# Kernel optimization log

Measured on AMD Instinct MI355X. Metric: run time of the kernel, lower is better.

The kernel has to match this reference:

```python
import jax, jax.numpy as jnp
import numpy as np
from itertools import product as _prod

B = 2          # batch size
NPB = 4096     # voxels per batch
C = 384        # input_dim
H = 8          # num_heads
OUT = 32       # output_dim (seg classes)
SPATIAL = (32, 256, 256)
POOL_R = np.array([1, 2, 2, 2])    # [1]+query_gs_ratio
COMP_R = np.array([1, 16, 16, 16])  # [1]+compress_ratio


def _coords():
    rng = np.random.default_rng(0)
    rows = []
    for b in range(B):
        cand = np.stack([rng.integers(0, s, 4 * NPB) for s in SPATIAL], 1)
        cand = np.unique(cand, axis=0)
        sel = cand[rng.permutation(len(cand))[:NPB]]
        rows.append(np.concatenate([np.full((NPB, 1), b, np.int64), sel], 1))
    return np.concatenate(rows).astype(np.int32)


def setup_inputs() -> dict:
    idx = _coords()                     # [N,4] unique (b,z,y,x)
    N = idx.shape[0]
    pool_u, pool_inv = np.unique(idx // POOL_R, axis=0, return_inverse=True)
    emb_u, emb_inv = np.unique(idx // COMP_R, axis=0, return_inverse=True)
    # submanifold 3x3x3 neighbor table (same batch), -1 = missing
    lut = {tuple(r): i for i, r in enumerate(idx.tolist())}
    nbr = np.full((N, 27), -1, np.int32)
    rows = idx.tolist()
    for k, (dz, dy, dx) in enumerate(_prod((-1, 0, 1), repeat=3)):
        for i, (b, z, y, x) in enumerate(rows):
            nbr[i, k] = lut.get((b, z + dz, y + dy, x + dx), -1)
    key = jax.random.key(0)
    ks = jax.random.split(key, 12)
    g = lambda k, shp, s: jax.random.normal(k, shp, jnp.float32) * s
    s = 1.0 / float(np.sqrt(C))
    return dict(
        feats=g(ks[0], (N, C), 1.0),
        W_pool=g(ks[1], (C, C), s), b_pool=jnp.zeros((C,), jnp.float32),
        W_emb=g(ks[2], (C, C), s), b_emb=jnp.zeros((C,), jnp.float32),
        Wq=g(ks[3], (C, C), s), bq=jnp.zeros((C,), jnp.float32),
        Wk=g(ks[4], (C, C), s), bk=jnp.zeros((C,), jnp.float32),
        Wv=g(ks[5], (C, C), s), bv=jnp.zeros((C,), jnp.float32),
        Wo=g(ks[6], (C, C), s), bo=jnp.zeros((C,), jnp.float32),
        W_conv=g(ks[7], (27, C, OUT), 1.0 / float(np.sqrt(27 * C))),
        b_conv=jnp.zeros((OUT,), jnp.float32),
        pool_inv=jnp.asarray(pool_inv, jnp.int32),
        pool_coords=jnp.asarray(pool_u, jnp.int32),
        emb_inv=jnp.asarray(emb_inv, jnp.int32),
        emb_coords=jnp.asarray(emb_u, jnp.int32),
        nbr_idx=jnp.asarray(nbr),
        batch_size=B,
    )


def _sine_pe(xyz, d_pos):
    # xyz: [n,3] normalized to [0,1]; PositionEmbeddingCoordsSine (3detr-style)
    cdim = d_pos // xyz.shape[1]
    dim_t = 10000.0 ** (2.0 * (jnp.arange(cdim) // 2).astype(jnp.float32) / cdim)
    emb = (xyz * (2.0 * jnp.pi))[:, :, None] / dim_t          # [n,3,cdim]
    pe = jnp.stack([jnp.sin(emb[..., 0::2]), jnp.cos(emb[..., 1::2])], -1)
    return pe.reshape(xyz.shape[0], -1)                        # [n,d_pos]


def reference(feats, W_pool, b_pool, W_emb, b_emb, Wq, bq, Wk, bk, Wv, bv,
              Wo, bo, W_conv, b_conv, pool_inv, pool_coords, emb_inv,
              emb_coords, nbr_idx, batch_size):
    Mp, Me, Cc = pool_coords.shape[0], emb_coords.shape[0], feats.shape[1]
    hd = Cc // H
    # query path: linear + scatter_max over pool cells
    pool_f = jax.ops.segment_max(feats @ W_pool + b_pool, pool_inv, num_segments=Mp)
    # kv path: linear + scatter_max over compressed cells (coords of argmax rows
    # within a cell all equal the unique cell coord, so mean == unique coord)
    emb_f = jax.ops.segment_max(feats @ W_emb + b_emb, emb_inv, num_segments=Me)
    # per-batch min/max-normalized sine positional encoding on concat(emb,pool)
    emb_xyz = emb_coords[:, 1:].astype(jnp.float32)
    pool_xyz = pool_coords[:, 1:].astype(jnp.float32)
    all_xyz = jnp.concatenate([emb_xyz, pool_xyz], 0)
    bids = jnp.concatenate([emb_coords[:, 0], pool_coords[:, 0]], 0)
    mins = jax.ops.segment_min(all_xyz, bids, num_segments=batch_size)
    maxs = jax.ops.segment_max(all_xyz, bids, num_segments=batch_size)
    norm = (all_xyz - mins[bids]) / (maxs[bids] - mins[bids] + 1e-6)
    pe = _sine_pe(norm, Cc)
    emb_f = emb_f + pe[:Me]
    pool_f = pool_f + pe[Me:]
    # multi-head cross-attention, masked to same-batch pairs
    q = (pool_f @ Wq + bq).reshape(Mp, H, hd)
    k = (emb_f @ Wk + bk).reshape(Me, H, hd)
    v = (emb_f @ Wv + bv).reshape(Me, H, hd)
    scores = jnp.einsum('phd,ehd->hpe', q, k) / jnp.sqrt(jnp.float32(hd))
    same_b = pool_coords[:, 0][None, :, None] == emb_coords[:, 0][None, None, :]
    attn = jax.nn.softmax(jnp.where(same_b, scores, -1e9), axis=-1)
    o = jnp.einsum('hpe,ehd->phd', attn, v).reshape(Mp, Cc) @ Wo + bo
    # broadcast back to voxels + residual
    new_f = feats + o[pool_inv]
    # SubMConv3d seg head: gather 27 neighbors, contract with kernel
    valid = (nbr_idx >= 0)[:, :, None]
    gathered = jnp.where(valid, new_f[jnp.maximum(nbr_idx, 0)], 0.0)  # [N,27,C]
    logits = jnp.einsum('nkc,kco->no', gathered, W_conv) + b_conv
    return logits
```

## Files before the change

### kernel.cpp

```cpp
#include <hip/hip_runtime.h>
#include <hip/hip_bf16.h>
#include <math.h>

#define CDIM 384
#define NHEAD 8
#define HD 48
#define OUTD 32
#define MAXB 16
#define CONVK 10368

typedef __bf16 bf16x8 __attribute__((ext_vector_type(8)));
typedef float f32x4 __attribute__((ext_vector_type(4)));

__device__ __forceinline__ f32x4 mfma16(bf16x8 a, bf16x8 b, f32x4 c) {
  return __builtin_amdgcn_mfma_f32_16x16x32_bf16(a, b, c, 0, 0, 0);
}
__device__ __forceinline__ bf16x8 zero8() {
  bf16x8 z = {(__bf16)0.f, (__bf16)0.f, (__bf16)0.f, (__bf16)0.f,
              (__bf16)0.f, (__bf16)0.f, (__bf16)0.f, (__bf16)0.f};
  return z;
}

__device__ __forceinline__ unsigned enc_f(float f) {
  unsigned u = __float_as_uint(f);
  return (u & 0x80000000u) ? ~u : (u | 0x80000000u);
}
__device__ __forceinline__ float dec_f(unsigned u) {
  unsigned v = (u & 0x80000000u) ? (u ^ 0x80000000u) : ~u;
  return __uint_as_float(v);
}

__global__ void init_small_kernel(int* smin, int* smax, int* eb) {
  int t = threadIdx.x;
  if (t < MAXB * 3) { smin[t] = 0x7fffffff; smax[t] = (int)0x80000000; }
  if (t <= MAXB) eb[t] = 0;
}

__global__ __launch_bounds__(256) void prep_kernel(
    const float* __restrict__ feats, __hip_bfloat16* __restrict__ feats16, int N,
    const float* __restrict__ W_pool, const float* __restrict__ W_emb,
    const float* __restrict__ Wk, const float* __restrict__ Wv,
    const float* __restrict__ Wq, const float* __restrict__ Wo,
    __hip_bfloat16* __restrict__ Wt_pe, __hip_bfloat16* __restrict__ Wt_kv,
    __hip_bfloat16* __restrict__ Wt_q, __hip_bfloat16* __restrict__ Wt_o,
    const float* __restrict__ Wc, __hip_bfloat16* __restrict__ Wct,
    unsigned* __restrict__ encA, unsigned* __restrict__ encB,
    __hip_bfloat16* __restrict__ vt, int Mepad,
    const int* __restrict__ ec, const int* __restrict__ pc, int Mp, int Me,
    const int* __restrict__ bsz, int* smin, int* smax, int* ebv,
    int nbF, int nbW, int nbC, int nbZA, int nbZB, int nbVt, int nbM) {
  __shared__ int lmin[MAXB * 3], lmax[MAXB * 3];
  int b = blockIdx.x;
  int t = threadIdx.x;
  if (b < nbF) {
    int v = b * 256 + t;
    if (v < N * 48) {
      float4 a0 = *reinterpret_cast<const float4*>(feats + (size_t)v * 8);
      float4 a1 = *reinterpret_cast<const float4*>(feats + (size_t)v * 8 + 4);
      __hip_bfloat16 tmp[8] = {
        __float2bfloat16(a0.x), __float2bfloat16(a0.y), __float2bfloat16(a0.z), __float2bfloat16(a0.w),
        __float2bfloat16(a1.x), __float2bfloat16(a1.y), __float2bfloat16(a1.z), __float2bfloat16(a1.w)};
      *reinterpret_cast<bf16x8*>(feats16 + (size_t)v * 8) = *reinterpret_cast<const bf16x8*>(tmp);
    }
    return;
  }
  b -= nbF;
  if (b < 6 * nbW) {
    int m = b / nbW;
    int v = (b - m * nbW) * 256 + t;
    if (v >= CDIM * 48) return;
    const float* src;
    __hip_bfloat16* dst;
    switch (m) {
      case 0: src = W_pool; dst = Wt_pe; break;
      case 1: src = W_emb;  dst = Wt_pe + (size_t)CDIM * CDIM; break;
      case 2: src = Wk;     dst = Wt_kv; break;
      case 3: src = Wv;     dst = Wt_kv + (size_t)CDIM * CDIM; break;
      case 4: src = Wq;     dst = Wt_q; break;
      default: src = Wo;    dst = Wt_o; break;
    }
    int k8i = v / CDIM;
    int n = v - k8i * CDIM;
    int k8 = k8i * 8;
    __hip_bfloat16 tmp[8];
    #pragma unroll
    for (int u = 0; u < 8; ++u) tmp[u] = __float2bfloat16(src[(size_t)(k8 + u) * CDIM + n]);
    *reinterpret_cast<bf16x8*>(dst + (size_t)n * CDIM + k8) = *reinterpret_cast<const bf16x8*>(tmp);
    return;
  }
  b -= 6 * nbW;
  if (b < nbC) {
    int v = b * 256 + t;
    if (v >= OUTD * (CONVK / 8)) return;
    int k8i = v >> 5;
    int n = v & 31;
    int k8 = k8i * 8;
    __hip_bfloat16 tmp[8];
    #pragma unroll
    for (int u = 0; u < 8; ++u) tmp[u] = __float2bfloat16(Wc[(size_t)(k8 + u) * OUTD + n]);
    *reinterpret_cast<bf16x8*>(Wct + (size_t)n * CONVK + k8) = *reinterpret_cast<const bf16x8*>(tmp);
    return;
  }
  b -= nbC;
  if (b < nbZA) {
    size_t v = (size_t)b * 256 + t;
    if (v < (size_t)Mp * 96) {
      uint4 z = {0u, 0u, 0u, 0u};
      reinterpret_cast<uint4*>(encA)[v] = z;
    }
    return;
  }
  b -= nbZA;
  if (b < nbZB) {
    size_t v = (size_t)b * 256 + t;
    if (v < (size_t)Me * 96) {
      uint4 z = {0u, 0u, 0u, 0u};
      reinterpret_cast<uint4*>(encB)[v] = z;
    }
    return;
  }
  b -= nbZB;
  if (b < nbVt) {
    int v = b * 256 + t;
    int g = Mepad >> 3;
    if (v < 512 * g) {
      int row = v / g;
      int c8 = (v - row * g) * 8;
      __hip_bfloat16 bv = __float2bfloat16(((row & 63) == HD) ? 1.0f : 0.0f);
      __hip_bfloat16 tmp[8] = {bv, bv, bv, bv, bv, bv, bv, bv};
      *reinterpret_cast<bf16x8*>(vt + (size_t)row * Mepad + c8) =
          *reinterpret_cast<const bf16x8*>(tmp);
    }
    return;
  }
  b -= nbVt;
  if (b < nbM) {
    if (t < MAXB * 3) { lmin[t] = 0x7fffffff; lmax[t] = (int)0x80000000; }
    __syncthreads();
    int i = b * 256 + t;
    int tot = Me + Mp;
    if (i < tot) {
      const int* r = (i < Me) ? (ec + 4 * i) : (pc + 4 * (i - Me));
      int bb = r[0];
      #pragma unroll
      for (int d = 0; d < 3; ++d) {
        atomicMin(&lmin[bb * 3 + d], r[1 + d]);
        atomicMax(&lmax[bb * 3 + d], r[1 + d]);
      }
    }
    __syncthreads();
    if (t < MAXB * 3) {
      if (lmin[t] != 0x7fffffff) atomicMin(&smin[t], lmin[t]);
      if (lmax[t] != (int)0x80000000) atomicMax(&smax[t], lmax[t]);
    }
    return;
  }
  b -= nbM;
  {
    int e = b * 256 + t;
    if (e == 0) { ebv[0] = 0; ebv[bsz[0]] = Me; }
    if (e > 0 && e < Me) {
      int b0 = ec[4 * (e - 1)], b1 = ec[4 * e];
      for (int bb = b0 + 1; bb <= b1; ++bb) ebv[bb] = e;
    }
  }
}

__global__ void pe_kernel(const unsigned* __restrict__ encP, const unsigned* __restrict__ encE,
                          __hip_bfloat16* __restrict__ pool16, __hip_bfloat16* __restrict__ emb16,
                          const int* __restrict__ pc, int Mp,
                          const int* __restrict__ ec, int Me,
                          const int* __restrict__ smin, const int* __restrict__ smax) {
  int gid = blockIdx.x * blockDim.x + threadIdx.x;
  int total = (Mp + Me) * CDIM;
  if (gid >= total) return;
  int row = gid / CDIM, c = gid - row * CDIM;
  const int* coords;
  const unsigned* src;
  __hip_bfloat16* dst;
  int lrow;
  if (row < Me) { lrow = row; coords = ec + 4 * row; src = encE; dst = emb16; }
  else { lrow = row - Me; coords = pc + 4 * lrow; src = encP; dst = pool16; }
  int b = coords[0];
  int dim = c >> 7;
  int i = c & 127;
  int j = i >> 1;
  float x = (float)coords[1 + dim];
  float mn = (float)smin[b * 3 + dim];
  float mx = (float)smax[b * 3 + dim];
  float nrm = (x - mn) / (mx - mn + 1e-6f);
  float freq = exp2f(-(float)j * 0.20762050593046014f);
  float arg = nrm * 6.283185307179586f * freq;
  float pe = (i & 1) ? __cosf(arg) : __sinf(arg);
  float val = dec_f(src[(size_t)lrow * CDIM + c]) + pe;
  dst[(size_t)lrow * CDIM + c] = __float2bfloat16(val);
}

template <int EPI>
__device__ __forceinline__ void mgemm_body(
    int bx, int by,
    __hip_bfloat16 (*As)[72], __hip_bfloat16 (*Bs)[72],
    const __hip_bfloat16* __restrict__ A, int M,
    const __hip_bfloat16* __restrict__ Wt,
    const float* __restrict__ bias0, const float* __restrict__ bias1,
    void* __restrict__ d0, void* __restrict__ d1,
    const int* __restrict__ inv0, const int* __restrict__ inv1,
    int Mepad) {
  const int m0 = bx * 128;
  const int n0 = by * 64;
  const int t = threadIdx.x;
  const int lane = t & 63, w = t >> 6;
  const int wr = w >> 1, wc = w & 1;
  const int lq = lane & 15, lg = lane >> 4;

  f32x4 acc[4][2];
  #pragma unroll
  for (int i = 0; i < 4; ++i) {
    acc[i][0] = (f32x4){0.f, 0.f, 0.f, 0.f};
    acc[i][1] = (f32x4){0.f, 0.f, 0.f, 0.f};
  }
  const int arow = t >> 3;
  const int acol = (t & 7) * 8;

  for (int k0 = 0; k0 < CDIM; k0 += 64) {
    #pragma unroll
    for (int i = 0; i < 4; ++i) {
      int r = arow + i * 32;
      int gr = m0 + r;
      bf16x8 val = zero8();
      if (gr < M) val = *reinterpret_cast<const bf16x8*>(A + (size_t)gr * CDIM + k0 + acol);
      *reinterpret_cast<bf16x8*>(&As[r][acol]) = val;
    }
    #pragma unroll
    for (int i = 0; i < 2; ++i) {
      int r = arow + i * 32;
      bf16x8 val = *reinterpret_cast<const bf16x8*>(Wt + (size_t)(n0 + r) * CDIM + k0 + acol);
      *reinterpret_cast<bf16x8*>(&Bs[r][acol]) = val;
    }
    __syncthreads();
    #pragma unroll
    for (int ks = 0; ks < 2; ++ks) {
      bf16x8 af[4], bfv[2];
      #pragma unroll
      for (int fm = 0; fm < 4; ++fm)
        af[fm] = *reinterpret_cast<const bf16x8*>(&As[wr * 64 + fm * 16 + lq][ks * 32 + lg * 8]);
      #pragma unroll
      for (int fn = 0; fn < 2; ++fn)
        bfv[fn] = *reinterpret_cast<const bf16x8*>(&Bs[wc * 32 + fn * 16 + lq][ks * 32 + lg * 8]);
      #pragma unroll
      for (int fm = 0; fm < 4; ++fm)
        #pragma unroll
        for (int fn = 0; fn < 2; ++fn)
          acc[fm][fn] = mfma16(af[fm], bfv[fn], acc[fm][fn]);
    }
    __syncthreads();
  }

  const bool sec = (n0 >= CDIM);
  const int nb = n0 - (sec ? CDIM : 0) + wc * 32;
  const int nA = nb + lq, nB = nb + 16 + lq;

  if (EPI == 0) {
    const float* bias = sec ? bias1 : bias0;
    unsigned* dst = (unsigned*)(sec ? d1 : d0);
    const int* inv = sec ? inv1 : inv0;
    float bA = bias[nA], bB = bias[nB];
    #pragma unroll
    for (int fm = 0; fm < 4; ++fm) {
      int rbase = m0 + wr * 64 + fm * 16 + lg * 4;
      int cs = -1;
      float mA = 0.f, mB = 0.f;
      #pragma unroll
      for (int j = 0; j < 4; ++j) {
        int r = rbase + j;
        if (r < M) {
          int s = inv[r];
          float vA = acc[fm][0][j] + bA;
          float vB = acc[fm][1][j] + bB;
          if (s == cs) { mA = fmaxf(mA, vA); mB = fmaxf(mB, vB); }
          else {
            if (cs >= 0) {
              atomicMax(&dst[(size_t)cs * CDIM + nA], enc_f(mA));
              atomicMax(&dst[(size_t)cs * CDIM + nB], enc_f(mB));
            }
            cs = s; mA = vA; mB = vB;
          }
        }
      }
      if (cs >= 0) {
        atomicMax(&dst[(size_t)cs * CDIM + nA], enc_f(mA));
        atomicMax(&dst[(size_t)cs * CDIM + nB], enc_f(mB));
      }
    }
  } else if (EPI == 1) {
    float bA = bias0[nA], bB = bias0[nB];
    float* dst = (float*)d0;
    #pragma unroll
    for (int fm = 0; fm < 4; ++fm)
      #pragma unroll
      for (int j = 0; j < 4; ++j) {
        int r = m0 + wr * 64 + fm * 16 + lg * 4 + j;
        if (r < M) {
          dst[(size_t)r * CDIM + nA] = acc[fm][0][j] + bA;
          dst[(size_t)r * CDIM + nB] = acc[fm][1][j] + bB;
        }
      }
  } else if (EPI == 2) {
    const float scale = 0.2082350914f;
    float bA = bias0[nA], bB = bias0[nB];
    int hA = nA / HD, dA = nA - hA * HD;
    int hB = nB / HD, dB = nB - hB * HD;
    __hip_bfloat16* dst = (__hip_bfloat16*)d0;
    #pragma unroll
    for (int fm = 0; fm < 4; ++fm)
      #pragma unroll
      for (int j = 0; j < 4; ++j) {
        int r = m0 + wr * 64 + fm * 16 + lg * 4 + j;
        if (r < M) {
          dst[(size_t)r * 512 + hA * 64 + dA] = __float2bfloat16((acc[fm][0][j] + bA) * scale);
          dst[(size_t)r * 512 + hB * 64 + dB] = __float2bfloat16((acc[fm][1][j] + bB) * scale);
        }
      }
  } else {
    if (!sec) {
      float bA = bias0[nA], bB = bias0[nB];
      int hA = nA / HD, dA = nA - hA * HD;
      int hB = nB / HD, dB = nB - hB * HD;
      __hip_bfloat16* dst = (__hip_bfloat16*)d0;
      #pragma unroll
      for (int fm = 0; fm < 4; ++fm)
        #pragma unroll
        for (int j = 0; j < 4; ++j) {
          int r = m0 + wr * 64 + fm * 16 + lg * 4 + j;
          if (r < M) {
            dst[(size_t)r * 512 + hA * 64 + dA] = __float2bfloat16(acc[fm][0][j] + bA);
            dst[(size_t)r * 512 + hB * 64 + dB] = __float2bfloat16(acc[fm][1][j] + bB);
          }
        }
    } else {
      float bA = bias1[nA], bB = bias1[nB];
      int hA = nA / HD, dA = nA - hA * HD;
      int hB = nB / HD, dB = nB - hB * HD;
      __hip_bfloat16* dst = (__hip_bfloat16*)d1;
      #pragma unroll
      for (int fm = 0; fm < 4; ++fm)
        #pragma unroll
        for (int j = 0; j < 4; ++j) {
          int r = m0 + wr * 64 + fm * 16 + lg * 4 + j;
          if (r < M) {
            dst[(size_t)(hA * 64 + dA) * Mepad + r] = __float2bfloat16(acc[fm][0][j] + bA);
            dst[(size_t)(hB * 64 + dB) * Mepad + r] = __float2bfloat16(acc[fm][1][j] + bB);
          }
        }
    }
  }
  if ((EPI == 2 || EPI == 3) && n0 == 0) {
    __hip_bfloat16* dst = (__hip_bfloat16*)d0;
    for (int c = t; c < 1024; c += 256) {
      int r = m0 + (c >> 3);
      int hx = c & 7;
      if (r < M) {
        bf16x8 z = zero8();
        *reinterpret_cast<bf16x8*>(dst + (size_t)r * 512 + hx * 64 + 48) = z;
        *reinterpret_cast<bf16x8*>(dst + (size_t)r * 512 + hx * 64 + 56) = z;
      }
    }
  }
}

__global__ __launch_bounds__(256) void mgemm0_kernel(
    const __hip_bfloat16* __restrict__ A, int M, const __hip_bfloat16* __restrict__ Wt,
    const float* __restrict__ bias0, const float* __restrict__ bias1,
    unsigned* __restrict__ d0, unsigned* __restrict__ d1,
    const int* __restrict__ inv0, const int* __restrict__ inv1) {
  __shared__ __align__(16) __hip_bfloat16 As[128][72];
  __shared__ __align__(16) __hip_bfloat16 Bs[64][72];
  mgemm_body<0>(blockIdx.x, blockIdx.y, As, Bs, A, M, Wt, bias0, bias1, d0, d1, inv0, inv1, 0);
}

__global__ __launch_bounds__(256) void mgemm1_kernel(
    const __hip_bfloat16* __restrict__ A, int M, const __hip_bfloat16* __restrict__ Wt,
    const float* __restrict__ bias0, float* __restrict__ d0) {
  __shared__ __align__(16) __hip_bfloat16 As[128][72];
  __shared__ __align__(16) __hip_bfloat16 Bs[64][72];
  mgemm_body<1>(blockIdx.x, blockIdx.y, As, Bs, A, M, Wt, bias0, nullptr, d0, nullptr, nullptr, nullptr, 0);
}

__global__ __launch_bounds__(256) void qkv_kernel(
    const __hip_bfloat16* __restrict__ pool16, int Mp, const __hip_bfloat16* __restrict__ Wt_q,
    const float* __restrict__ bq,
    const __hip_bfloat16* __restrict__ emb16, int Me, const __hip_bfloat16* __restrict__ Wt_kv,
    const float* __restrict__ bk, const float* __restrict__ bv,
    __hip_bfloat16* __restrict__ q16, __hip_bfloat16* __restrict__ k16,
    __hip_bfloat16* __restrict__ vt, int Mepad, int nbQ, int gxQ, int gxK) {
  __shared__ __align__(16) __hip_bfloat16 As[128][72];
  __shared__ __align__(16) __hip_bfloat16 Bs[64][72];
  int b = blockIdx.x;
  if (b < nbQ) {
    mgemm_body<2>(b % gxQ, b / gxQ, As, Bs, pool16, Mp, Wt_q, bq, nullptr,
                  q16, nullptr, nullptr, nullptr, 0);
  } else {
    b -= nbQ;
    mgemm_body<3>(b % gxK, b / gxK, As, Bs, emb16, Me, Wt_kv, bk, bv,
                  k16, vt, nullptr, nullptr, Mepad);
  }
}

__global__ __launch_bounds__(512) void attn_mfma_kernel(
    const __hip_bfloat16* __restrict__ qb, const __hip_bfloat16* __restrict__ kb,
    const __hip_bfloat16* __restrict__ vt, int Mepad,
    const int* __restrict__ pc, const int* __restrict__ eb,
    int Mp, int Me, __hip_bfloat16* __restrict__ ob) {
  __shared__ __align__(16) __hip_bfloat16 Ks[2][64][72];
  __shared__ __align__(16) __hip_bfloat16 Vs[2][64][72];
  __shared__ __align__(16) __hip_bfloat16 pl[8][16][72];
  __shared__ int sred[8][4];
  const int h = blockIdx.y;
  const int t = threadIdx.x;
  const int wv = t >> 6, lane = t & 63;
  const int lq = lane & 15, lg = lane >> 4;
  const int q0 = blockIdx.x * 128 + wv * 16;

  int lo[4], hi[4];
  #pragma unroll
  for (int r = 0; r < 4; ++r) {
    int q = q0 + lg * 4 + r;
    if (q < Mp) { int b = pc[4 * q]; lo[r] = eb[b]; hi[r] = eb[b + 1]; }
    else { lo[r] = 0x7fffffff; hi[r] = 0; }
  }
  int lomin = min(min(lo[0], lo[1]), min(lo[2], lo[3]));
  int lomax = max(max(lo[0], lo[1]), max(lo[2], lo[3]));
  int himin = min(min(hi[0], hi[1]), min(hi[2], hi[3]));
  int himax = max(max(hi[0], hi[1]), max(hi[2], hi[3]));
  #pragma unroll
  for (int off = 1; off < 64; off <<= 1) {
    lomin = min(lomin, __shfl_xor(lomin, off));
    lomax = max(lomax, __shfl_xor(lomax, off));
    himin = min(himin, __shfl_xor(himin, off));
    himax = max(himax, __shfl_xor(himax, off));
  }
  if (lane == 0) {
    sred[wv][0] = lomin; sred[wv][1] = lomax;
    sred[wv][2] = himin; sred[wv][3] = himax;
  }
  __syncthreads();
  #pragma unroll
  for (int i = 0; i < 8; ++i) {
    lomin = min(lomin, sred[i][0]);
    lomax = max(lomax, sred[i][1]);
    himin = min(himin, sred[i][2]);
    himax = max(himax, sred[i][3]);
  }

  int qrow = min(q0 + lq, Mp - 1);
  const __hip_bfloat16* qp = qb + (size_t)qrow * 512 + h * 64 + lg * 8;
  bf16x8 aq0 = *reinterpret_cast<const bf16x8*>(qp);
  bf16x8 aq1 = *reinterpret_cast<const bf16x8*>(qp + 32);

  const int str = t >> 3;
  const int stc = (t & 7) * 8;
  const __hip_bfloat16* vrow = vt + (size_t)(h * 64 + str) * Mepad + stc;

  f32x4 zero = {0.f, 0.f, 0.f, 0.f};
  f32x4 oacc[4];
  oacc[0] = zero; oacc[1] = zero; oacc[2] = zero; oacc[3] = zero;

  bf16x8 k0, v0;
  auto load_tile = [&](int e0) {
    int er = e0 + str;
    k0 = zero8();
    if (er < Me)
      k0 = *reinterpret_cast<const bf16x8*>(kb + (size_t)er * 512 + h * 64 + stc);
    v0 = *reinterpret_cast<const bf16x8*>(vrow + e0);
  };
  auto store_tile = [&](int nb) {
    *reinterpret_cast<bf16x8*>(&Ks[nb][str][stc]) = k0;
    *reinterpret_cast<bf16x8*>(&Vs[nb][str][stc]) = v0;
  };
  const int e0beg = lomin & ~63;
  load_tile(e0beg);
  store_tile(0);
  if (e0beg + 64 < himax) load_tile(e0beg + 64);

  int it = 0;
  for (int e0 = e0beg; e0 < himax; e0 += 64, ++it) {
    __syncthreads();
    const int cur = it & 1;
    if (e0 + 64 < himax) {
      store_tile(cur ^ 1);
      if (e0 + 128 < himax) load_tile(e0 + 128);
    }

    f32x4 sf[4];
    #pragma unroll
    for (int s = 0; s < 4; ++s) {
      bf16x8 bk0 = *reinterpret_cast<const bf16x8*>(&Ks[cur][s * 16 + lq][lg * 8]);
      bf16x8 bk1 = *reinterpret_cast<const bf16x8*>(&Ks[cur][s * 16 + lq][32 + lg * 8]);
      f32x4 z = zero;
      z = mfma16(aq0, bk0, z);
      z = mfma16(aq1, bk1, z);
      sf[s] = z;
    }
    const bool interior = (e0 >= lomax) && (e0 + 64 <= himin);
    if (interior) {
      #pragma unroll
      for (int s = 0; s < 4; ++s)
        #pragma unroll
        for (int r = 0; r < 4; ++r)
          pl[wv][lg * 4 + r][s * 16 + lq] = __float2bfloat16(exp2f(sf[s][r]));
    } else {
      #pragma unroll
      for (int s = 0; s < 4; ++s) {
        int e = e0 + s * 16 + lq;
        #pragma unroll
        for (int r = 0; r < 4; ++r) {
          bool m = (e >= lo[r]) && (e < hi[r]);
          float p = m ? exp2f(sf[s][r]) : 0.f;
          pl[wv][lg * 4 + r][s * 16 + lq] = __float2bfloat16(p);
        }
      }
    }
    asm volatile("s_waitcnt lgkmcnt(0)" ::: "memory");
    __builtin_amdgcn_sched_barrier(0);
    #pragma unroll
    for (int ks = 0; ks < 2; ++ks) {
      bf16x8 ap = *reinterpret_cast<const bf16x8*>(&pl[wv][lq][ks * 32 + lg * 8]);
      #pragma unroll
      for (int dt = 0; dt < 4; ++dt) {
        bf16x8 bv = *reinterpret_cast<const bf16x8*>(&Vs[cur][dt * 16 + lq][ks * 32 + lg * 8]);
        oacc[dt] = mfma16(ap, bv, oacc[dt]);
      }
    }
  }

  #pragma unroll
  for (int r = 0; r < 4; ++r) {
    float l = __shfl(oacc[3][r], (lane & 48));
    int q = q0 + lg * 4 + r;
    if (q < Mp && l > 0.f) {
      float inv = 1.0f / l;
      __hip_bfloat16* op = ob + (size_t)q * CDIM + h * HD;
      op[lq]      = __float2bfloat16(oacc[0][r] * inv);
      op[16 + lq] = __float2bfloat16(oacc[1][r] * inv);
      op[32 + lq] = __float2bfloat16(oacc[2][r] * inv);
    }
  }
}

__global__ void newf16_kernel(const float* __restrict__ feats, const float* __restrict__ o2,
                              const int* __restrict__ pinv, __hip_bfloat16* __restrict__ nf,
                              int N) {
  int v = blockIdx.x * 256 + threadIdx.x;
  if (v >= N * 48) return;
  int n = v / 48, c8 = (v - n * 48) * 8;
  const float* fp = feats + (size_t)n * CDIM + c8;
  const float* op = o2 + (size_t)pinv[n] * CDIM + c8;
  float4 a0 = *reinterpret_cast<const float4*>(fp);
  float4 a1 = *reinterpret_cast<const float4*>(fp + 4);
  float4 b0 = *reinterpret_cast<const float4*>(op);
  float4 b1 = *reinterpret_cast<const float4*>(op + 4);
  __hip_bfloat16 tmp[8] = {
    __float2bfloat16(a0.x + b0.x), __float2bfloat16(a0.y + b0.y),
    __float2bfloat16(a0.z + b0.z), __float2bfloat16(a0.w + b0.w),
    __float2bfloat16(a1.x + b1.x), __float2bfloat16(a1.y + b1.y),
    __float2bfloat16(a1.z + b1.z), __float2bfloat16(a1.w + b1.w)};
  *reinterpret_cast<bf16x8*>(nf + (size_t)v * 8) = *reinterpret_cast<const bf16x8*>(tmp);
}

__global__ __launch_bounds__(256) void mconv_kernel(
    const __hip_bfloat16* __restrict__ nf, const int* __restrict__ nbr,
    const __hip_bfloat16* __restrict__ Wct, float* __restrict__ outp, int N) {
  __shared__ __align__(16) __hip_bfloat16 As[128][72];
  __shared__ __align__(16) __hip_bfloat16 Bs[32][72];
  __shared__ int jrow[128];
  const int n0 = blockIdx.x * 128;
  const int kg = blockIdx.y;
  const int t = threadIdx.x;
  const int lane = t & 63, w = t >> 6;
  const int lq = lane & 15, lg = lane >> 4;
  f32x4 acc[2][2];
  acc[0][0] = (f32x4){0.f,0.f,0.f,0.f}; acc[0][1] = acc[0][0];
  acc[1][0] = acc[0][0]; acc[1][1] = acc[0][0];
  const int arow = t >> 3, acol = (t & 7) * 8;

  for (int kk = kg * 3; kk < kg * 3 + 3; ++kk) {
    __syncthreads();
    if (t < 128) {
      int n = n0 + t;
      jrow[t] = (n < N) ? nbr[(size_t)n * 27 + kk] : -1;
    }
    __syncthreads();
    for (int c0 = 0; c0 < CDIM; c0 += 64) {
      #pragma unroll
      for (int i = 0; i < 4; ++i) {
        int r = arow + i * 32;
        int j = jrow[r];
        bf16x8 val = zero8();
        if (j >= 0) val = *reinterpret_cast<const bf16x8*>(nf + (size_t)j * CDIM + c0 + acol);
        *reinterpret_cast<bf16x8*>(&As[r][acol]) = val;
      }
      {
        int r = t >> 3;
        bf16x8 val = *reinterpret_cast<const bf16x8*>(Wct + (size_t)r * CONVK + kk * CDIM + c0 + acol);
        *reinterpret_cast<bf16x8*>(&Bs[r][acol]) = val;
      }
      __syncthreads();
      #pragma unroll
      for (int ks = 0; ks < 2; ++ks) {
        bf16x8 af[2], bfv[2];
        #pragma unroll
        for (int fm = 0; fm < 2; ++fm)
          af[fm] = *reinterpret_cast<const bf16x8*>(&As[w * 32 + fm * 16 + lq][ks * 32 + lg * 8]);
        #pragma unroll
        for (int fn = 0; fn < 2; ++fn)
          bfv[fn] = *reinterpret_cast<const bf16x8*>(&Bs[fn * 16 + lq][ks * 32 + lg * 8]);
        #pragma unroll
        for (int fm = 0; fm < 2; ++fm)
          #pragma unroll
          for (int fn = 0; fn < 2; ++fn)
            acc[fm][fn] = mfma16(af[fm], bfv[fn], acc[fm][fn]);
      }
      __syncthreads();
    }
  }
  #pragma unroll
  for (int fm = 0; fm < 2; ++fm)
    #pragma unroll
    for (int j = 0; j < 4; ++j) {
      int r = n0 + w * 32 + fm * 16 + lg * 4 + j;
      if (r < N) {
        #pragma unroll
        for (int fn = 0; fn < 2; ++fn)
          outp[((size_t)kg * N + r) * OUTD + fn * 16 + lq] = acc[fm][fn][j];
      }
    }
}

__global__ void conv_reduce_kernel(const float* __restrict__ outp,
                                   const float* __restrict__ bc,
                                   float* __restrict__ out, int N) {
  int v = blockIdx.x * 256 + threadIdx.x;
  if (v >= N * OUTD) return;
  int oo = v & (OUTD - 1);
  float s = bc[oo];
  #pragma unroll
  for (int kg = 0; kg < 9; ++kg) s += outp[(size_t)kg * N * OUTD + v];
  out[v] = s;
}

extern "C" void kernel_launch(void* const* d_in, const int* in_sizes, int n_in,
                              void* d_out, int out_size, void* d_ws, size_t ws_size,
                              hipStream_t stream) {
  const float* feats  = (const float*)d_in[0];
  const float* W_pool = (const float*)d_in[1];
  const float* b_pool = (const float*)d_in[2];
  const float* W_emb  = (const float*)d_in[3];
  const float* b_emb  = (const float*)d_in[4];
  const float* Wq = (const float*)d_in[5];  const float* bq = (const float*)d_in[6];
  const float* Wk = (const float*)d_in[7];  const float* bk = (const float*)d_in[8];
  const float* Wv = (const float*)d_in[9];  const float* bv = (const float*)d_in[10];
  const float* Wo = (const float*)d_in[11]; const float* bo = (const float*)d_in[12];
  const float* Wc = (const float*)d_in[13]; const float* bc = (const float*)d_in[14];
  const int* pool_inv    = (const int*)d_in[15];
  const int* pool_coords = (const int*)d_in[16];
  const int* emb_inv     = (const int*)d_in[17];
  const int* emb_coords  = (const int*)d_in[18];
  const int* nbr         = (const int*)d_in[19];
  const int* bsz         = (const int*)d_in[20];
  int N  = in_sizes[0] / CDIM;
  int Mp = in_sizes[16] / 4;
  int Me = in_sizes[18] / 4;
  int Mepad = ((Me >> 6) + 2) << 6;

  char* wsb = (char*)d_ws;
  size_t off = 0;
  auto alloc = [&](size_t bytes) { void* p = wsb + off; off += (bytes + 255) & ~(size_t)255; return p; };
  unsigned* encA = (unsigned*)alloc((size_t)Mp * CDIM * 4);
  unsigned* encB = (unsigned*)alloc((size_t)Me * CDIM * 4);
  __hip_bfloat16* vt = (__hip_bfloat16*)alloc((size_t)512 * Mepad * 2);
  __hip_bfloat16* pool16  = (__hip_bfloat16*)alloc((size_t)Mp * CDIM * 2);
  __hip_bfloat16* emb16   = (__hip_bfloat16*)alloc((size_t)Me * CDIM * 2);
  __hip_bfloat16* feats16 = (__hip_bfloat16*)alloc((size_t)N * CDIM * 2);
  float* o2 = (float*)alloc((size_t)Mp * CDIM * 4 > (size_t)9 * N * OUTD * 4
                                ? (size_t)Mp * CDIM * 4 : (size_t)9 * N * OUTD * 4);
  __hip_bfloat16* Wt_pe = (__hip_bfloat16*)alloc((size_t)768 * CDIM * 2);
  __hip_bfloat16* Wt_kv = (__hip_bfloat16*)alloc((size_t)768 * CDIM * 2);
  __hip_bfloat16* Wt_q  = (__hip_bfloat16*)alloc((size_t)CDIM * CDIM * 2);
  __hip_bfloat16* Wt_o  = (__hip_bfloat16*)alloc((size_t)CDIM * CDIM * 2);
  __hip_bfloat16* Wct   = (__hip_bfloat16*)alloc((size_t)OUTD * CONVK * 2);
  int* smin = (int*)alloc(MAXB * 3 * 4);
  int* smax = (int*)alloc(MAXB * 3 * 4);
  int* eb   = (int*)alloc((MAXB + 1) * 4);

  __hip_bfloat16* q16  = (__hip_bfloat16*)encA;
  __hip_bfloat16* k16  = (__hip_bfloat16*)encB;
  __hip_bfloat16* ob16 = pool16;
  __hip_bfloat16* newf16 = feats16;
  float* outp = o2;

  init_small_kernel<<<1, 64, 0, stream>>>(smin, smax, eb);

  int nbF  = (N * 48 + 255) / 256;
  int nbW  = (CDIM * 48 + 255) / 256;
  int nbC  = (OUTD * (CONVK / 8) + 255) / 256;
  int nbZA = ((Mp * 96) + 255) / 256;
  int nbZB = ((Me * 96) + 255) / 256;
  int nbVt = ((512 * (Mepad >> 3)) + 255) / 256;
  int nbM  = (Mp + Me + 255) / 256;
  int nbE  = (Me + 255) / 256;
  prep_kernel<<<nbF + 6 * nbW + nbC + nbZA + nbZB + nbVt + nbM + nbE, 256, 0, stream>>>(
      feats, feats16, N, W_pool, W_emb, Wk, Wv, Wq, Wo,
      Wt_pe, Wt_kv, Wt_q, Wt_o, Wc, Wct, encA, encB, vt, Mepad,
      emb_coords, pool_coords, Mp, Me, bsz, smin, smax, eb,
      nbF, nbW, nbC, nbZA, nbZB, nbVt, nbM);

  mgemm0_kernel<<<dim3((N + 127) / 128, 12), 256, 0, stream>>>(
      feats16, N, Wt_pe, b_pool, b_emb, encA, encB, pool_inv, emb_inv);
  pe_kernel<<<((Mp + Me) * CDIM + 255) / 256, 256, 0, stream>>>(
      encA, encB, pool16, emb16, pool_coords, Mp, emb_coords, Me, smin, smax);

  {
    int gxQ = (Mp + 127) / 128, gxK = (Me + 127) / 128;
    int nbQ = gxQ * 6;
    qkv_kernel<<<nbQ + gxK * 12, 256, 0, stream>>>(
        pool16, Mp, Wt_q, bq, emb16, Me, Wt_kv, bk, bv,
        q16, k16, vt, Mepad, nbQ, gxQ, gxK);
  }

  attn_mfma_kernel<<<dim3((Mp + 127) / 128, NHEAD), 512, 0, stream>>>(
      q16, k16, vt, Mepad, pool_coords, eb, Mp, Me, ob16);

  mgemm1_kernel<<<dim3((Mp + 127) / 128, 6), 256, 0, stream>>>(
      ob16, Mp, Wt_o, bo, o2);

  newf16_kernel<<<(N * 48 + 255) / 256, 256, 0, stream>>>(feats, o2, pool_inv, newf16, N);

  mconv_kernel<<<dim3((N + 127) / 128, 9), 256, 0, stream>>>(newf16, nbr, Wct, outp, N);
  conv_reduce_kernel<<<(N * OUTD + 255) / 256, 256, 0, stream>>>(outp, bc, (float*)d_out, N);
}
```

Before: 164.0 us.

## Read K/V straight from global in head-major layout, drop LDS staging

The K projection now writes its output head-major ([head][row][64]) so each head's keys are contiguous. The attention kernel no longer stages K and V tiles through double-buffered shared memory with block-wide barriers; each wave loads its MFMA operands directly from global memory and uses its own batch range instead of a block-wide reduction. Blocks shrink to 64 queries and 256 threads. This removes barrier and LDS-copy overhead, but the waves in a block no longer share K/V data, which increases global/L2 traffic and exposes load latency in the inner loop.

```diff
diff --git a/kernel.cpp b/kernel.cpp
--- a/kernel.cpp
+++ b/kernel.cpp
@@ -333,8 +333,8 @@
         for (int j = 0; j < 4; ++j) {
           int r = m0 + wr * 64 + fm * 16 + lg * 4 + j;
           if (r < M) {
-            dst[(size_t)r * 512 + hA * 64 + dA] = __float2bfloat16(acc[fm][0][j] + bA);
-            dst[(size_t)r * 512 + hB * 64 + dB] = __float2bfloat16(acc[fm][1][j] + bB);
+            dst[((size_t)hA * Mepad + r) * 64 + dA] = __float2bfloat16(acc[fm][0][j] + bA);
+            dst[((size_t)hB * Mepad + r) * 64 + dB] = __float2bfloat16(acc[fm][1][j] + bB);
           }
         }
     } else {
@@ -354,7 +354,7 @@
         }
     }
   }
-  if ((EPI == 2 || EPI == 3) && n0 == 0) {
+  if (EPI == 2 && n0 == 0) {
     __hip_bfloat16* dst = (__hip_bfloat16*)d0;
     for (int c = t; c < 1024; c += 256) {
       int r = m0 + (c >> 3);
@@ -366,6 +366,18 @@
       }
     }
   }
+  if (EPI == 3 && n0 == 0) {
+    __hip_bfloat16* dst = (__hip_bfloat16*)d0;
+    for (int c = t; c < 1024; c += 256) {
+      int r = m0 + (c >> 3);
+      int hx = c & 7;
+      if (r < M) {
+        bf16x8 z = zero8();
+        *reinterpret_cast<bf16x8*>(dst + ((size_t)hx * Mepad + r) * 64 + 48) = z;
+        *reinterpret_cast<bf16x8*>(dst + ((size_t)hx * Mepad + r) * 64 + 56) = z;
+      }
+    }
+  }
 }
 
 __global__ __launch_bounds__(256) void mgemm0_kernel(
@@ -391,35 +403,32 @@
     const float* __restrict__ bq,
     const __hip_bfloat16* __restrict__ emb16, int Me, const __hip_bfloat16* __restrict__ Wt_kv,
     const float* __restrict__ bk, const float* __restrict__ bv,
-    __hip_bfloat16* __restrict__ q16, __hip_bfloat16* __restrict__ k16,
+    __hip_bfloat16* __restrict__ q16, __hip_bfloat16* __restrict__ kf,
     __hip_bfloat16* __restrict__ vt, int Mepad, int nbQ, int gxQ, int gxK) {
   __shared__ __align__(16) __hip_bfloat16 As[128][72];
   __shared__ __align__(16) __hip_bfloat16 Bs[64][72];
   int b = blockIdx.x;
   if (b < nbQ) {
     mgemm_body<2>(b % gxQ, b / gxQ, As, Bs, pool16, Mp, Wt_q, bq, nullptr,
-                  q16, nullptr, nullptr, nullptr, 0);
+                  q16, nullptr, nullptr, nullptr, Mepad);
   } else {
     b -= nbQ;
     mgemm_body<3>(b % gxK, b / gxK, As, Bs, emb16, Me, Wt_kv, bk, bv,
-                  k16, vt, nullptr, nullptr, Mepad);
-  }
-}
-
-__global__ __launch_bounds__(512) void attn_mfma_kernel(
-    const __hip_bfloat16* __restrict__ qb, const __hip_bfloat16* __restrict__ kb,
+                  kf, vt, nullptr, nullptr, Mepad);
+  }
+}
+
+__global__ __launch_bounds__(256) void attn_mfma_kernel(
+    const __hip_bfloat16* __restrict__ qb, const __hip_bfloat16* __restrict__ kf,
     const __hip_bfloat16* __restrict__ vt, int Mepad,
     const int* __restrict__ pc, const int* __restrict__ eb,
     int Mp, int Me, __hip_bfloat16* __restrict__ ob) {
-  __shared__ __align__(16) __hip_bfloat16 Ks[2][64][72];
-  __shared__ __align__(16) __hip_bfloat16 Vs[2][64][72];
-  __shared__ __align__(16) __hip_bfloat16 pl[8][16][72];
-  __shared__ int sred[8][4];
+  __shared__ __align__(16) __hip_bfloat16 pl[4][16][72];
   const int h = blockIdx.y;
   const int t = threadIdx.x;
   const int wv = t >> 6, lane = t & 63;
   const int lq = lane & 15, lg = lane >> 4;
-  const int q0 = blockIdx.x * 128 + wv * 16;
+  const int q0 = blockIdx.x * 64 + wv * 16;
 
   int lo[4], hi[4];
   #pragma unroll
@@ -439,63 +448,26 @@
     himin = min(himin, __shfl_xor(himin, off));
     himax = max(himax, __shfl_xor(himax, off));
   }
-  if (lane == 0) {
-    sred[wv][0] = lomin; sred[wv][1] = lomax;
-    sred[wv][2] = himin; sred[wv][3] = himax;
-  }
-  __syncthreads();
-  #pragma unroll
-  for (int i = 0; i < 8; ++i) {
-    lomin = min(lomin, sred[i][0]);
-    lomax = max(lomax, sred[i][1]);
-    himin = min(himin, sred[i][2]);
-    himax = max(himax, sred[i][3]);
-  }
 
   int qrow = min(q0 + lq, Mp - 1);
   const __hip_bfloat16* qp = qb + (size_t)qrow * 512 + h * 64 + lg * 8;
   bf16x8 aq0 = *reinterpret_cast<const bf16x8*>(qp);
   bf16x8 aq1 = *reinterpret_cast<const bf16x8*>(qp + 32);
 
-  const int str = t >> 3;
-  const int stc = (t & 7) * 8;
-  const __hip_bfloat16* vrow = vt + (size_t)(h * 64 + str) * Mepad + stc;
+  const __hip_bfloat16* kbase = kf + (size_t)h * Mepad * 64;
+  const __hip_bfloat16* vbase = vt + (size_t)h * 64 * Mepad;
 
   f32x4 zero = {0.f, 0.f, 0.f, 0.f};
   f32x4 oacc[4];
   oacc[0] = zero; oacc[1] = zero; oacc[2] = zero; oacc[3] = zero;
 
-  bf16x8 k0, v0;
-  auto load_tile = [&](int e0) {
-    int er = e0 + str;
-    k0 = zero8();
-    if (er < Me)
-      k0 = *reinterpret_cast<const bf16x8*>(kb + (size_t)er * 512 + h * 64 + stc);
-    v0 = *reinterpret_cast<const bf16x8*>(vrow + e0);
-  };
-  auto store_tile = [&](int nb) {
-    *reinterpret_cast<bf16x8*>(&Ks[nb][str][stc]) = k0;
-    *reinterpret_cast<bf16x8*>(&Vs[nb][str][stc]) = v0;
-  };
-  const int e0beg = lomin & ~63;
-  load_tile(e0beg);
-  store_tile(0);
-  if (e0beg + 64 < himax) load_tile(e0beg + 64);
-
-  int it = 0;
-  for (int e0 = e0beg; e0 < himax; e0 += 64, ++it) {
-    __syncthreads();
-    const int cur = it & 1;
-    if (e0 + 64 < himax) {
-      store_tile(cur ^ 1);
-      if (e0 + 128 < himax) load_tile(e0 + 128);
-    }
-
+  for (int e0 = (lomin & ~63); e0 < himax; e0 += 64) {
     f32x4 sf[4];
     #pragma unroll
     for (int s = 0; s < 4; ++s) {
-      bf16x8 bk0 = *reinterpret_cast<const bf16x8*>(&Ks[cur][s * 16 + lq][lg * 8]);
-      bf16x8 bk1 = *reinterpret_cast<const bf16x8*>(&Ks[cur][s * 16 + lq][32 + lg * 8]);
+      const __hip_bfloat16* kp = kbase + (size_t)(e0 + s * 16 + lq) * 64 + lg * 8;
+      bf16x8 bk0 = *reinterpret_cast<const bf16x8*>(kp);
+      bf16x8 bk1 = *reinterpret_cast<const bf16x8*>(kp + 32);
       f32x4 z = zero;
       z = mfma16(aq0, bk0, z);
       z = mfma16(aq1, bk1, z);
@@ -527,7 +499,8 @@
       bf16x8 ap = *reinterpret_cast<const bf16x8*>(&pl[wv][lq][ks * 32 + lg * 8]);
       #pragma unroll
       for (int dt = 0; dt < 4; ++dt) {
-        bf16x8 bv = *reinterpret_cast<const bf16x8*>(&Vs[cur][dt * 16 + lq][ks * 32 + lg * 8]);
+        const __hip_bfloat16* vp = vbase + (size_t)(dt * 16 + lq) * Mepad + e0 + ks * 32 + lg * 8;
+        bf16x8 bv = *reinterpret_cast<const bf16x8*>(vp);
         oacc[dt] = mfma16(ap, bv, oacc[dt]);
       }
     }
@@ -692,8 +665,8 @@
   int* smax = (int*)alloc(MAXB * 3 * 4);
   int* eb   = (int*)alloc((MAXB + 1) * 4);
 
-  __hip_bfloat16* q16  = (__hip_bfloat16*)encA;
-  __hip_bfloat16* k16  = (__hip_bfloat16*)encB;
+  __hip_bfloat16* q16 = (__hip_bfloat16*)encA;
+  __hip_bfloat16* kf  = (__hip_bfloat16*)encB;
   __hip_bfloat16* ob16 = pool16;
   __hip_bfloat16* newf16 = feats16;
   float* outp = o2;
@@ -724,11 +697,11 @@
     int nbQ = gxQ * 6;
     qkv_kernel<<<nbQ + gxK * 12, 256, 0, stream>>>(
         pool16, Mp, Wt_q, bq, emb16, Me, Wt_kv, bk, bv,
-        q16, k16, vt, Mepad, nbQ, gxQ, gxK);
-  }
-
-  attn_mfma_kernel<<<dim3((Mp + 127) / 128, NHEAD), 512, 0, stream>>>(
-      q16, k16, vt, Mepad, pool_coords, eb, Mp, Me, ob16);
+        q16, kf, vt, Mepad, nbQ, gxQ, gxK);
+  }
+
+  attn_mfma_kernel<<<dim3((Mp + 63) / 64, NHEAD), 256, 0, stream>>>(
+      q16, kf, vt, Mepad, pool_coords, eb, Mp, Me, ob16);
 
   mgemm1_kernel<<<dim3((Mp + 127) / 128, 6), 256, 0, stream>>>(
       ob16, Mp, Wt_o, bo, o2);
```

Result: slower. 202.6 us (+23.5%).
